# Performance work log

Measured on AMD Instinct MI355X. Metric: run time of the kernel, lower is better.

## Reference

```python
import jax, jax.numpy as jnp
import numpy as np

R = 16
ALPHA = 32.0
SCALING = ALPHA / max(1, R)

def setup_inputs() -> dict:
    key = jax.random.key(0)
    ks = jax.random.split(key, 7)
    B_, D, M = 16384, 1024, 4096
    return {
        "x": jax.random.normal(ks[0], (B_, D), dtype=jnp.float32),
        "W0": jax.random.normal(ks[1], (M, D), dtype=jnp.float32) * 0.02,
        "b0": jax.random.normal(ks[2], (M,), dtype=jnp.float32) * 0.02,
        "A": jax.random.normal(ks[3], (R, D), dtype=jnp.float32) * 0.001,
        "B": jax.random.normal(ks[4], (M, R), dtype=jnp.float32) * 0.02,
        "W2": jax.random.normal(ks[5], (1, M), dtype=jnp.float32) * 0.02,
        "b2": jax.random.normal(ks[6], (1,), dtype=jnp.float32) * 0.02,
    }

def reference(x, W0, b0, A, B, W2, b2):
    # effective_W = W0 + scaling * (B @ A)  -> [m_hidden, d_in]
    W_eff = W0 + SCALING * (B @ A)
    # F.linear(x, W_eff, b0): x @ W_eff^T + b0 -> [batch, m_hidden]
    h = jax.nn.relu(jnp.einsum('bd,md->bm', x, W_eff) + b0)
    # fc2: [batch, 1] then squeeze(-1)
    out = (jnp.einsum('bm,om->bo', h, W2) + b2).squeeze(-1)
    return out
```

## Files before the change

### kernel.cpp

```cpp
#include <hip/hip_runtime.h>
#include <hip/hip_bf16.h>
#include <stdint.h>

#define BATCH  16384
#define D_IN   1024
#define M_HID  4096
#define R_LORA 16
#define SCALING 2.0f


typedef __bf16 bf16x8 __attribute__((ext_vector_type(8)));
typedef float  f32x16 __attribute__((ext_vector_type(16)));

__device__ __forceinline__ unsigned f2bf(float f) {
    union { float f; unsigned u; } c; c.f = f;
    unsigned u = c.u;
    return ((u + 0x7FFFu + ((u >> 16) & 1u)) >> 16);
}

__global__ __launch_bounds__(256) void k_wprep(
    const float* __restrict__ W0, const float* __restrict__ A,
    const float* __restrict__ Bl, unsigned short* __restrict__ wb)
{
    int id = blockIdx.x * 256 + threadIdx.x;
    int rl  = id & 31;
    int c   = (id >> 5) & 127;
    int n32 = id >> 12;
    int n = n32 * 32 + rl, k0 = c * 8;
    const float* wr = W0 + (size_t)n * D_IN + k0;
    float4 v0 = *(const float4*)(wr);
    float4 v1 = *(const float4*)(wr + 4);
    const float* brow = Bl + n * R_LORA;
    float4 bb[4];
    bb[0] = *(const float4*)(brow);
    bb[1] = *(const float4*)(brow + 4);
    bb[2] = *(const float4*)(brow + 8);
    bb[3] = *(const float4*)(brow + 12);
    const float bs[16] = { bb[0].x, bb[0].y, bb[0].z, bb[0].w,
                           bb[1].x, bb[1].y, bb[1].z, bb[1].w,
                           bb[2].x, bb[2].y, bb[2].z, bb[2].w,
                           bb[3].x, bb[3].y, bb[3].z, bb[3].w };
#pragma unroll
    for (int r = 0; r < R_LORA; ++r) {
        float s = SCALING * bs[r];
        const float* ar = A + r * D_IN + k0;
        float4 a0 = *(const float4*)(ar);
        float4 a1 = *(const float4*)(ar + 4);
        v0.x += s * a0.x; v0.y += s * a0.y; v0.z += s * a0.z; v0.w += s * a0.w;
        v1.x += s * a1.x; v1.y += s * a1.y; v1.z += s * a1.z; v1.w += s * a1.w;
    }
    uint4 o;
    o.x = f2bf(v0.x) | (f2bf(v0.y) << 16);
    o.y = f2bf(v0.z) | (f2bf(v0.w) << 16);
    o.z = f2bf(v1.x) | (f2bf(v1.y) << 16);
    o.w = f2bf(v1.z) | (f2bf(v1.w) << 16);
    ((uint4*)wb)[id] = o;
}

__global__ __launch_bounds__(1024, 4) void k_strip(
    const float* __restrict__ xf, const unsigned short* __restrict__ wb,
    const float* __restrict__ b0, const float* __restrict__ W2,
    const float* __restrict__ b2, float* __restrict__ out)
{
    __shared__ unsigned short As[64 * 1024];
    __shared__ float red[16][64];

    const int tid  = threadIdx.x;
    const int lane = tid & 63;
    const int wave = tid >> 6;
    const int rl   = lane & 31;
    const int half = lane >> 5;
    const int row0 = blockIdx.x * 64;

    ((float*)red)[tid] = 0.f;

    {
        const int so8 = tid & 127;
        const int rb  = tid >> 7;
        const float* xsrc = xf + (size_t)row0 * D_IN + so8 * 8;
#pragma unroll
        for (int j = 0; j < 8; ++j) {
            const int r = j * 8 + rb;
            const float* p = xsrc + (size_t)r * D_IN;
            float4 v0 = *(const float4*)(p);
            float4 v1 = *(const float4*)(p + 4);
            uint4 o;
            o.x = f2bf(v0.x) | (f2bf(v0.y) << 16);
            o.y = f2bf(v0.z) | (f2bf(v0.w) << 16);
            o.z = f2bf(v1.x) | (f2bf(v1.y) << 16);
            o.w = f2bf(v1.z) | (f2bf(v1.w) << 16);
            *(uint4*)(&As[r * 1024 + ((so8 ^ (r & 31)) << 3)]) = o;
        }
    }
    __syncthreads();

    for (int pass = 0; pass < 4; ++pass) {
        const int n0 = pass * 1024 + wave * 64;
        const float w2a = W2[n0 + rl],      b0a = b0[n0 + rl];
        const float w2b = W2[n0 + 32 + rl], b0b = b0[n0 + 32 + rl];
        const int n32 = n0 >> 5;
        const unsigned short* w0p = wb + (size_t)n32 * 32768 + half * 256 + rl * 8;
        const unsigned short* w1p = w0p + 32768;

        f32x16 acc[2][2] = {};
        bf16x8 wf0[4], wf1[4];
#pragma unroll
        for (int p = 0; p < 4; ++p) {
            wf0[p] = *(const bf16x8*)(w0p + p * 512);
            wf1[p] = *(const bf16x8*)(w1p + p * 512);
        }

#pragma unroll 4
        for (int kk = 0; kk < 60; ++kk) {
            const int cur = kk & 3;
            const int oc  = kk * 2 + half;
            bf16x8 af0 = *(const bf16x8*)(&As[rl * 1024 + ((oc ^ rl) << 3)]);
            bf16x8 af1 = *(const bf16x8*)(&As[(32 + rl) * 1024 + ((oc ^ rl) << 3)]);
            bf16x8 w0c = wf0[cur], w1c = wf1[cur];
            wf0[cur] = *(const bf16x8*)(w0p + (kk + 4) * 512);
            wf1[cur] = *(const bf16x8*)(w1p + (kk + 4) * 512);
            acc[0][0] = __builtin_amdgcn_mfma_f32_32x32x16_bf16(af0, w0c, acc[0][0], 0, 0, 0);
            acc[0][1] = __builtin_amdgcn_mfma_f32_32x32x16_bf16(af0, w1c, acc[0][1], 0, 0, 0);
            acc[1][0] = __builtin_amdgcn_mfma_f32_32x32x16_bf16(af1, w0c, acc[1][0], 0, 0, 0);
            acc[1][1] = __builtin_amdgcn_mfma_f32_32x32x16_bf16(af1, w1c, acc[1][1], 0, 0, 0);
        }
#pragma unroll
        for (int kk = 60; kk < 64; ++kk) {
            const int cur = kk & 3;
            const int oc  = kk * 2 + half;
            bf16x8 af0 = *(const bf16x8*)(&As[rl * 1024 + ((oc ^ rl) << 3)]);
            bf16x8 af1 = *(const bf16x8*)(&As[(32 + rl) * 1024 + ((oc ^ rl) << 3)]);
            acc[0][0] = __builtin_amdgcn_mfma_f32_32x32x16_bf16(af0, wf0[cur], acc[0][0], 0, 0, 0);
            acc[0][1] = __builtin_amdgcn_mfma_f32_32x32x16_bf16(af0, wf1[cur], acc[0][1], 0, 0, 0);
            acc[1][0] = __builtin_amdgcn_mfma_f32_32x32x16_bf16(af1, wf0[cur], acc[1][0], 0, 0, 0);
            acc[1][1] = __builtin_amdgcn_mfma_f32_32x32x16_bf16(af1, wf1[cur], acc[1][1], 0, 0, 0);
        }

#pragma unroll
        for (int ti = 0; ti < 2; ++ti)
#pragma unroll
            for (int r = 0; r < 16; ++r) {
                float p = fmaxf(acc[ti][0][r] + b0a, 0.f) * w2a
                        + fmaxf(acc[ti][1][r] + b0b, 0.f) * w2b;
#pragma unroll
                for (int m = 1; m <= 16; m <<= 1)
                    p += __shfl_xor(p, m, 64);
                if (rl == 0)
                    red[wave][ti * 32 + (r & 3) + 8 * (r >> 2) + 4 * half] += p;
            }
    }

    __syncthreads();
    if (tid < 64) {
        float s = b2[0];
#pragma unroll
        for (int w = 0; w < 16; ++w) s += red[w][tid];
        out[row0 + tid] = s;
    }
}

__global__ __launch_bounds__(256) void k_naive(
    const float* __restrict__ x, const float* __restrict__ W0,
    const float* __restrict__ b0, const float* __restrict__ A,
    const float* __restrict__ Bl, const float* __restrict__ W2,
    const float* __restrict__ b2, float* __restrict__ out)
{
    __shared__ float xs[D_IN];
    int b = blockIdx.x;
    for (int d = threadIdx.x; d < D_IN; d += 256) xs[d] = x[(size_t)b * D_IN + d];
    __syncthreads();
    float part = 0.f;
    for (int m = threadIdx.x; m < M_HID; m += 256) {
        float h = b0[m];
        const float* wr = W0 + (size_t)m * D_IN;
        const float* brow = Bl + m * R_LORA;
        for (int d = 0; d < D_IN; ++d) {
            float w = wr[d];
            for (int r = 0; r < R_LORA; ++r) w += SCALING * brow[r] * A[r * D_IN + d];
            h += xs[d] * w;
        }
        part += fmaxf(h, 0.f) * W2[m];
    }
    __shared__ float sred[256];
    sred[threadIdx.x] = part;
    __syncthreads();
    for (int s = 128; s > 0; s >>= 1) {
        if (threadIdx.x < s) sred[threadIdx.x] += sred[threadIdx.x + s];
        __syncthreads();
    }
    if (threadIdx.x == 0) out[b] = sred[0] + b2[0];
}

extern "C" void kernel_launch(void* const* d_in, const int* in_sizes, int n_in,
                              void* d_out, int out_size, void* d_ws, size_t ws_size,
                              hipStream_t stream) {
    const float* x  = (const float*)d_in[0];
    const float* W0 = (const float*)d_in[1];
    const float* b0 = (const float*)d_in[2];
    const float* A  = (const float*)d_in[3];
    const float* Bl = (const float*)d_in[4];
    const float* W2 = (const float*)d_in[5];
    const float* b2 = (const float*)d_in[6];
    float* out = (float*)d_out;

    const size_t wb_bytes = (size_t)M_HID * D_IN * 2;
    if (ws_size >= wb_bytes) {
        unsigned short* wb = (unsigned short*)d_ws;
        hipLaunchKernelGGL(k_wprep, dim3(M_HID * D_IN / 8 / 256), dim3(256), 0, stream,
                           W0, A, Bl, wb);
        hipLaunchKernelGGL(k_strip, dim3(BATCH / 64), dim3(1024), 0, stream,
                           x, wb, b0, W2, b2, out);
    } else {
        hipLaunchKernelGGL(k_naive, dim3(BATCH), dim3(256), 0, stream,
                           x, W0, b0, A, Bl, W2, b2, out);
    }
}
```

Measured before the change: 267.1 us.

## Split hidden dimension across two blocks per strip and coalesce weight prep

The main GEMM kernel now uses 512-thread blocks, each covering one 64-row strip and half of the hidden dimension, for 512 blocks instead of 256. Partial fc2 sums are combined with atomicAdd into an output that a new init kernel pre-fills with the bias. The weight-prep kernel is also restructured: it loads the LoRA B rows into shared memory and reads W0 rows with coalesced accesses. The split improves occupancy and load balance across CUs, but each x strip is now converted to bf16 twice and float atomics make the summation order nondeterministic.

```diff
diff --git a/kernel.cpp b/kernel.cpp
--- a/kernel.cpp
+++ b/kernel.cpp
@@ -18,59 +18,73 @@
     return ((u + 0x7FFFu + ((u >> 16) & 1u)) >> 16);
 }
 
-__global__ __launch_bounds__(256) void k_wprep(
+__global__ __launch_bounds__(512) void k_wprep(
     const float* __restrict__ W0, const float* __restrict__ A,
     const float* __restrict__ Bl, unsigned short* __restrict__ wb)
 {
-    int id = blockIdx.x * 256 + threadIdx.x;
-    int rl  = id & 31;
-    int c   = (id >> 5) & 127;
-    int n32 = id >> 12;
-    int n = n32 * 32 + rl, k0 = c * 8;
-    const float* wr = W0 + (size_t)n * D_IN + k0;
-    float4 v0 = *(const float4*)(wr);
-    float4 v1 = *(const float4*)(wr + 4);
-    const float* brow = Bl + n * R_LORA;
-    float4 bb[4];
-    bb[0] = *(const float4*)(brow);
-    bb[1] = *(const float4*)(brow + 4);
-    bb[2] = *(const float4*)(brow + 8);
-    bb[3] = *(const float4*)(brow + 12);
-    const float bs[16] = { bb[0].x, bb[0].y, bb[0].z, bb[0].w,
-                           bb[1].x, bb[1].y, bb[1].z, bb[1].w,
-                           bb[2].x, bb[2].y, bb[2].z, bb[2].w,
-                           bb[3].x, bb[3].y, bb[3].z, bb[3].w };
-#pragma unroll
-    for (int r = 0; r < R_LORA; ++r) {
-        float s = SCALING * bs[r];
-        const float* ar = A + r * D_IN + k0;
-        float4 a0 = *(const float4*)(ar);
-        float4 a1 = *(const float4*)(ar + 4);
-        v0.x += s * a0.x; v0.y += s * a0.y; v0.z += s * a0.z; v0.w += s * a0.w;
-        v1.x += s * a1.x; v1.y += s * a1.y; v1.z += s * a1.z; v1.w += s * a1.w;
-    }
-    uint4 o;
-    o.x = f2bf(v0.x) | (f2bf(v0.y) << 16);
-    o.y = f2bf(v0.z) | (f2bf(v0.w) << 16);
-    o.z = f2bf(v1.x) | (f2bf(v1.y) << 16);
-    o.w = f2bf(v1.z) | (f2bf(v1.w) << 16);
-    ((uint4*)wb)[id] = o;
-}
-
-__global__ __launch_bounds__(1024, 4) void k_strip(
+    __shared__ float Bs[512];
+    const int tid   = threadIdx.x;
+    const int n32   = blockIdx.x >> 1;
+    const int chalf = blockIdx.x & 1;
+    const int col0  = chalf * 512;
+
+    Bs[tid] = SCALING * Bl[n32 * 512 + tid];
+    __syncthreads();
+
+    const int lane = tid & 63;
+    const int w    = tid >> 6;
+    const float* a_base = A + col0 + lane * 8;
+
+#pragma unroll
+    for (int j = 0; j < 4; ++j) {
+        const int row = j * 8 + w;
+        const int n   = n32 * 32 + row;
+        const float* p = W0 + (size_t)n * D_IN + col0 + lane * 8;
+        float4 v0 = *(const float4*)(p);
+        float4 v1 = *(const float4*)(p + 4);
+        const float* bsr = &Bs[row * 16];
+#pragma unroll
+        for (int r = 0; r < R_LORA; ++r) {
+            float s = bsr[r];
+            const float* ap = a_base + r * D_IN;
+            float4 a0 = *(const float4*)(ap);
+            float4 a1 = *(const float4*)(ap + 4);
+            v0.x += s * a0.x; v0.y += s * a0.y; v0.z += s * a0.z; v0.w += s * a0.w;
+            v1.x += s * a1.x; v1.y += s * a1.y; v1.z += s * a1.z; v1.w += s * a1.w;
+        }
+        uint4 o;
+        o.x = f2bf(v0.x) | (f2bf(v0.y) << 16);
+        o.y = f2bf(v0.z) | (f2bf(v0.w) << 16);
+        o.z = f2bf(v1.x) | (f2bf(v1.y) << 16);
+        o.w = f2bf(v1.z) | (f2bf(v1.w) << 16);
+        *(uint4*)(&wb[(size_t)n32 * 32768 + (size_t)(chalf * 64 + lane) * 256 + row * 8]) = o;
+    }
+}
+
+__global__ __launch_bounds__(256) void k_init(
+    const float* __restrict__ b2, float* __restrict__ out)
+{
+    out[blockIdx.x * 256 + threadIdx.x] = b2[0];
+}
+
+__global__ __launch_bounds__(512, 2) void k_strip(
     const float* __restrict__ xf, const unsigned short* __restrict__ wb,
     const float* __restrict__ b0, const float* __restrict__ W2,
-    const float* __restrict__ b2, float* __restrict__ out)
+    float* __restrict__ out)
 {
     __shared__ unsigned short As[64 * 1024];
-    __shared__ float red[16][64];
+    __shared__ float red[8][64];
 
     const int tid  = threadIdx.x;
     const int lane = tid & 63;
     const int wave = tid >> 6;
     const int rl   = lane & 31;
     const int half = lane >> 5;
-    const int row0 = blockIdx.x * 64;
+
+    const int bid   = blockIdx.x;
+    const int mhalf = (bid >> 2) & 1;
+    const int strip = (bid & 3) | ((bid >> 3) << 2);
+    const int row0  = strip * 64;
 
     ((float*)red)[tid] = 0.f;
 
@@ -79,8 +93,8 @@
         const int rb  = tid >> 7;
         const float* xsrc = xf + (size_t)row0 * D_IN + so8 * 8;
 #pragma unroll
-        for (int j = 0; j < 8; ++j) {
-            const int r = j * 8 + rb;
+        for (int j = 0; j < 16; ++j) {
+            const int r = j * 4 + rb;
             const float* p = xsrc + (size_t)r * D_IN;
             float4 v0 = *(const float4*)(p);
             float4 v1 = *(const float4*)(p + 4);
@@ -95,7 +109,7 @@
     __syncthreads();
 
     for (int pass = 0; pass < 4; ++pass) {
-        const int n0 = pass * 1024 + wave * 64;
+        const int n0 = mhalf * 2048 + pass * 512 + wave * 64;
         const float w2a = W2[n0 + rl],      b0a = b0[n0 + rl];
         const float w2b = W2[n0 + 32 + rl], b0b = b0[n0 + 32 + rl];
         const int n32 = n0 >> 5;
@@ -152,10 +166,10 @@
 
     __syncthreads();
     if (tid < 64) {
-        float s = b2[0];
-#pragma unroll
-        for (int w = 0; w < 16; ++w) s += red[w][tid];
-        out[row0 + tid] = s;
+        float s = 0.f;
+#pragma unroll
+        for (int w = 0; w < 8; ++w) s += red[w][tid];
+        atomicAdd(&out[row0 + tid], s);
     }
 }
 
@@ -206,10 +220,12 @@
     const size_t wb_bytes = (size_t)M_HID * D_IN * 2;
     if (ws_size >= wb_bytes) {
         unsigned short* wb = (unsigned short*)d_ws;
-        hipLaunchKernelGGL(k_wprep, dim3(M_HID * D_IN / 8 / 256), dim3(256), 0, stream,
+        hipLaunchKernelGGL(k_wprep, dim3(M_HID / 32 * 2), dim3(512), 0, stream,
                            W0, A, Bl, wb);
-        hipLaunchKernelGGL(k_strip, dim3(BATCH / 64), dim3(1024), 0, stream,
-                           x, wb, b0, W2, b2, out);
+        hipLaunchKernelGGL(k_init, dim3(BATCH / 256), dim3(256), 0, stream,
+                           b2, out);
+        hipLaunchKernelGGL(k_strip, dim3(512), dim3(512), 0, stream,
+                           x, wb, b0, W2, out);
     } else {
         hipLaunchKernelGGL(k_naive, dim3(BATCH), dim3(256), 0, stream,
                            x, W0, b0, A, Bl, W2, b2, out);
```

Result: slower. 355.0 us (+32.9%).
